# Performance work log

Measured on AMD Instinct MI355X. Metric: run time of the kernel, lower is better.

Reference implementation:

```python
import math
import jax, jax.numpy as jnp
import numpy as np

D_MODEL = 512
MAX_SEQ = 512
NUM_OUT = 16
H = 1  # num_heads


def _pos_encoding(d_model, seq_len):
    # sinusoidal PE, then flipped along the sequence axis (ReversedPositionalEncoding)
    pos = jnp.arange(seq_len, dtype=jnp.float32)[:, None]
    i = jnp.arange(0, d_model, 2, dtype=jnp.float32)
    ang = pos * jnp.exp(i * (-(math.log(10000.0) / d_model)))  # [S, d/2]
    pe = jnp.stack([jnp.sin(ang), jnp.cos(ang)], axis=-1).reshape(seq_len, d_model)
    return pe[::-1]


def _layernorm(x, w, b, eps=1e-5):
    m = jnp.mean(x, axis=-1, keepdims=True)
    v = jnp.mean(jnp.square(x - m), axis=-1, keepdims=True)
    return (x - m) / jnp.sqrt(v + eps) * w + b


def setup_inputs() -> dict:
    key = jax.random.key(0)
    ks = jax.random.split(key, 8)
    B = 128
    latents = jax.random.normal(ks[0], (B, D_MODEL, MAX_SEQ), dtype=jnp.float32)
    query_mask = jnp.ones((B, NUM_OUT), dtype=jnp.float32)
    query = 0.02 * jax.random.normal(ks[1], (NUM_OUT, D_MODEL), dtype=jnp.float32)
    return {
        "latents": latents,
        "query_mask": query_mask,
        "query": query,
        "ln_lat_w": jnp.ones((D_MODEL,), jnp.float32),
        "ln_lat_b": jnp.zeros((D_MODEL,), jnp.float32),
        "ln_q_w": jnp.ones((D_MODEL,), jnp.float32),
        "ln_q_b": jnp.zeros((D_MODEL,), jnp.float32),
        "Wq": 0.02 * jax.random.normal(ks[2], (D_MODEL, D_MODEL), jnp.float32),
        "bq": jnp.zeros((D_MODEL,), jnp.float32),
        "Wk": 0.02 * jax.random.normal(ks[3], (D_MODEL, D_MODEL), jnp.float32),
        "bk": jnp.zeros((D_MODEL,), jnp.float32),
        "Wv": 0.02 * jax.random.normal(ks[4], (D_MODEL, D_MODEL), jnp.float32),
        "bv": jnp.zeros((D_MODEL,), jnp.float32),
        "Wo": 0.02 * jax.random.normal(ks[5], (1, D_MODEL), jnp.float32),
        "bo": jnp.zeros((1,), jnp.float32),
    }


def reference(latents, query_mask, query, ln_lat_w, ln_lat_b, ln_q_w, ln_q_b,
              Wq, bq, Wk, bk, Wv, bv, Wo, bo):
    B, _, N = latents.shape  # latents: [B, d_model, N]
    scale = math.sqrt(D_MODEL)
    Dh = D_MODEL // H

    # cross-attention mask: query_mask [B,Nq] x all-ones latent mask [B,N]
    mask = jnp.einsum('bq,bk->bqk', query_mask, jnp.ones((B, N), latents.dtype))

    x = jnp.swapaxes(latents, 1, 2) * scale           # [B, N, d]
    x = x + _pos_encoding(D_MODEL, MAX_SEQ)[-N:]      # reversed PE, last N positions
    # dropout is identity in eval mode
    x = _layernorm(x, ln_lat_w, ln_lat_b)

    q = _layernorm(query * scale, ln_q_w, ln_q_b)     # [Nq, d]
    q = jnp.broadcast_to(q[None], (B, NUM_OUT, D_MODEL))

    qh = (q @ Wq.T + bq).reshape(B, NUM_OUT, H, Dh)
    kh = (x @ Wk.T + bk).reshape(B, N, H, Dh)
    vh = (x @ Wv.T + bv).reshape(B, N, H, Dh)

    scores = jnp.einsum('bqhd,bkhd->bhqk', qh, kh) / math.sqrt(Dh)
    scores = jnp.where(mask[:, None] == 0, -1e9, scores)
    attn_weights = jax.nn.softmax(scores, axis=-1)    # [B, H, Nq, N]

    attn = jnp.einsum('bhqk,bkhd->bqhd', attn_weights, vh).reshape(B, NUM_OUT, H * Dh)
    wipe = jnp.all(mask == 0, axis=2, keepdims=True)  # [B, Nq, 1]
    attn = jnp.where(wipe, 0.0, attn)

    logits = attn @ Wo.T + bo                         # [B, Nq, 1]
    return logits, attn_weights
```

## Files before the change

### kernel.cpp

```cpp
#include <hip/hip_runtime.h>
#include <math.h>

#define DM 512
#define NQ 16
#define NG (NQ + 1)
#define NR (NG + 3)

typedef __attribute__((ext_vector_type(2))) float f32x2;

__device__ __forceinline__ float wave_reduce_sum(float v) {
    #pragma unroll
    for (int off = 32; off > 0; off >>= 1) v += __shfl_xor(v, off, 64);
    return v;
}
__device__ __forceinline__ float wave_reduce_max(float v) {
    #pragma unroll
    for (int off = 32; off > 0; off >>= 1) v = fmaxf(v, __shfl_xor(v, off, 64));
    return v;
}

__global__ void k1_setup(const float* __restrict__ Wk, const float* __restrict__ Wv,
                         const float* __restrict__ query,
                         const float* __restrict__ ln_q_w, const float* __restrict__ ln_q_b,
                         float* __restrict__ PET, float* __restrict__ WkT,
                         float* __restrict__ WvT, float* __restrict__ q_ln, int N) {
    __shared__ float tile[64][65];
    int bx = blockIdx.x;
    int lane = threadIdx.x & 63;
    int w = threadIdx.x >> 6;

    if (bx < 128) {
        int ntile = bx & 7, jg = bx >> 3;
        int n = ntile * 64 + lane;
        float p = (float)(N - 1 - n);
        const float c = -logf(10000.f) / (float)DM;
        int jbase = jg * 16 + w * 4;
        #pragma unroll
        for (int u = 0; u < 4; ++u) {
            int j = jbase + u;
            float wj = expf((float)(2 * j) * c);
            float ang = p * wj;
            PET[(size_t)(2 * j) * N + n] = sinf(ang);
            PET[(size_t)(2 * j + 1) * N + n] = cosf(ang);
        }
    } else if (bx < 256) {
        int t = bx - 128;
        const float* W = (t >> 6) ? Wv : Wk;
        float* WT = (t >> 6) ? WvT : WkT;
        int tl = t & 63;
        int te = tl >> 3, td = tl & 7;
        #pragma unroll
        for (int i = 0; i < 16; ++i) {
            int el = w * 16 + i;
            tile[el][lane] = W[(size_t)(te * 64 + el) * DM + td * 64 + lane];
        }
        __syncthreads();
        #pragma unroll
        for (int i = 0; i < 16; ++i) {
            int dl = w * 16 + i;
            WT[(size_t)(td * 64 + dl) * DM + te * 64 + lane] = tile[lane][dl];
        }
    } else {
        const float scale = 22.627416997969522f;
        for (int qi = 0; qi < 4; ++qi) {
            int q = w * 4 + qi;
            float vals[8], s = 0.f, s2 = 0.f;
            #pragma unroll
            for (int i = 0; i < 8; ++i) {
                float x = query[q * DM + i * 64 + lane] * scale;
                vals[i] = x; s += x; s2 += x * x;
            }
            s = wave_reduce_sum(s); s2 = wave_reduce_sum(s2);
            float m = s * (1.f / DM);
            float var = s2 * (1.f / DM) - m * m;
            float rstd = rsqrtf(var + 1e-5f);
            #pragma unroll
            for (int i = 0; i < 8; ++i) {
                int d = i * 64 + lane;
                q_ln[q * DM + d] = (vals[i] - m) * rstd * ln_q_w[d] + ln_q_b[d];
            }
        }
    }
}

__global__ void k2_qh(const float* __restrict__ q_ln, const float* __restrict__ Wq,
                      const float* __restrict__ bq, float* __restrict__ qh) {
    int idx = blockIdx.x * 4 + (threadIdx.x >> 6);
    int lane = threadIdx.x & 63;
    int q = idx >> 9, e = idx & 511;
    const float4* wr = (const float4*)(Wq + (size_t)e * DM);
    const float4* xr = (const float4*)(q_ln + (size_t)q * DM);
    float4 w0 = wr[lane * 2], w1 = wr[lane * 2 + 1];
    float4 x0 = xr[lane * 2], x1 = xr[lane * 2 + 1];
    float s = w0.x * x0.x + w0.y * x0.y + w0.z * x0.z + w0.w * x0.w
            + w1.x * x1.x + w1.y * x1.y + w1.z * x1.z + w1.w * x1.w;
    s = wave_reduce_sum(s);
    if (lane == 0) qh[q * DM + e] = s + bq[e];
}

__global__ void k3_qt(const float* __restrict__ qh, const float* __restrict__ WkT,
                      const float* __restrict__ Wo, const float* __restrict__ WvT,
                      const float* __restrict__ lnw,
                      float* __restrict__ qt, float* __restrict__ A,
                      f32x2* __restrict__ A2, float* __restrict__ wvout) {
    int idx = blockIdx.x * 4 + (threadIdx.x >> 6);
    int lane = threadIdx.x & 63;
    int g = idx >> 9, d = idx & 511;
    const float4* wr;
    const float4* xr;
    if (g < NQ) {
        wr = (const float4*)(WkT + (size_t)d * DM);
        xr = (const float4*)(qh + (size_t)g * DM);
    } else {
        wr = (const float4*)(WvT + (size_t)d * DM);
        xr = (const float4*)Wo;
    }
    float4 w0 = wr[lane * 2], w1 = wr[lane * 2 + 1];
    float4 x0 = xr[lane * 2], x1 = xr[lane * 2 + 1];
    float s = w0.x * x0.x + w0.y * x0.y + w0.z * x0.z + w0.w * x0.w
            + w1.x * x1.x + w1.y * x1.y + w1.z * x1.z + w1.w * x1.w;
    s = wave_reduce_sum(s);
    if (lane == 0) {
        if (g < NQ) qt[g * DM + d] = s;
        else wvout[d] = s;
        float a = s * lnw[d];
        A[g * DM + d] = a;
        f32x2 ap; ap.x = a; ap.y = a;
        A2[g * DM + d] = ap;
    }
}

__global__ void k4_pea(const float* __restrict__ A, const float* __restrict__ PET,
                       const float* __restrict__ qt, const float* __restrict__ qh,
                       const float* __restrict__ wv, const float* __restrict__ lnb,
                       const float* __restrict__ bk, const float* __restrict__ Wo,
                       const float* __restrict__ bv,
                       float* __restrict__ peA, float* __restrict__ peS,
                       float* __restrict__ peQ, float* __restrict__ consts, int N) {
    __shared__ float red[4][64];
    int bx = blockIdx.x;
    int lane = threadIdx.x & 63;
    int w = threadIdx.x >> 6;

    if (bx < 152) {
        int g = bx >> 3, ntile = bx & 7;
        int n = ntile * 64 + lane;
        int d0 = w * 128;
        float acc = 0.f;
        if (g < NG) {
            for (int i = 0; i < 128; ++i) {
                int d = d0 + i;
                acc = fmaf(A[(size_t)g * DM + d], PET[(size_t)d * N + n], acc);
            }
        } else if (g == NG) {
            for (int i = 0; i < 128; ++i) acc += PET[(size_t)(d0 + i) * N + n];
        } else {
            for (int i = 0; i < 128; ++i) {
                float v = PET[(size_t)(d0 + i) * N + n];
                acc = fmaf(v, v, acc);
            }
        }
        red[w][lane] = acc;
        __syncthreads();
        if (w != 0) return;
        float tot = red[0][lane] + red[1][lane] + red[2][lane] + red[3][lane];
        if (g < NG) peA[(size_t)g * N + n] = tot;
        else if (g == NG) peS[n] = tot;
        else peQ[n] = tot;
    } else {
        int t = (bx - 152) * 4 + w;
        if (t > NQ) return;
        if (t < NQ) {
            float sa = 0.f, sc = 0.f, qb = 0.f;
            #pragma unroll
            for (int i = 0; i < 8; ++i) {
                int d = i * 64 + lane;
                sa += A[t * DM + d];
                sc = fmaf(qt[t * DM + d], lnb[d], sc);
                qb = fmaf(qh[t * DM + d], bk[d], qb);
            }
            sa = wave_reduce_sum(sa);
            sc = wave_reduce_sum(sc);
            qb = wave_reduce_sum(qb);
            if (lane == 0) { consts[t] = sa; consts[16 + t] = sc + qb; }
        } else {
            float sa = 0.f, cv = 0.f, bvo = 0.f;
            #pragma unroll
            for (int i = 0; i < 8; ++i) {
                int d = i * 64 + lane;
                sa += A[NQ * DM + d];
                cv = fmaf(wv[d], lnb[d], cv);
                bvo = fmaf(Wo[d], bv[d], bvo);
            }
            sa = wave_reduce_sum(sa);
            cv = wave_reduce_sum(cv);
            bvo = wave_reduce_sum(bvo);
            if (lane == 0) { consts[32] = sa; consts[33] = cv + bvo; }
        }
    }
}

__launch_bounds__(256, 4)
__global__ void main2_kernel(const float* __restrict__ latents,
                             const float* __restrict__ PET,
                             const f32x2* __restrict__ A2,
                             float* __restrict__ pbuf, int N) {
    int ntiles = N >> 7;
    int ntile = blockIdx.x % ntiles;
    int dh = blockIdx.x / ntiles;
    int b = blockIdx.y;
    int lane = threadIdx.x & 63;
    int w = threadIdx.x >> 6;
    int n0 = ntile * 128 + lane * 2;

    int d0 = __builtin_amdgcn_readfirstlane(dh * 256 + w * 64);
    const float* latf = latents + (size_t)b * DM * N + (size_t)d0 * N + n0;
    const float* petf = PET + (size_t)d0 * N + n0;

    f32x2 acc[NG];
    #pragma unroll
    for (int i = 0; i < NG; ++i) { acc[i].x = 0.f; acc[i].y = 0.f; }
    f32x2 S1 = {0.f, 0.f}, S2 = {0.f, 0.f}, Sx = {0.f, 0.f};

    const int U = 4;
    const int NC = 64 / U;
    f32x2 xb[2][U], pb[2][U];
    #pragma unroll
    for (int u = 0; u < U; ++u) {
        xb[0][u] = __builtin_nontemporal_load((const f32x2*)(latf + (size_t)u * N));
        pb[0][u] = *(const f32x2*)(petf + (size_t)u * N);
    }
    for (int c = 0; c < NC; c += 2) {
        #pragma unroll
        for (int u = 0; u < U; ++u) {
            size_t dd = (size_t)((c + 1) * U + u) * N;
            xb[1][u] = __builtin_nontemporal_load((const f32x2*)(latf + dd));
            pb[1][u] = *(const f32x2*)(petf + dd);
        }
        #pragma unroll
        for (int u = 0; u < U; ++u) {
            f32x2 x = xb[0][u], pe = pb[0][u];
            S1 += x; S2 += x * x; Sx += x * pe;
            int d = d0 + c * U + u;
            #pragma unroll
            for (int q = 0; q < NG; ++q)
                acc[q] += A2[(size_t)q * DM + d] * x;
        }
        if (c + 2 < NC) {
            #pragma unroll
            for (int u = 0; u < U; ++u) {
                size_t dd = (size_t)((c + 2) * U + u) * N;
                xb[0][u] = __builtin_nontemporal_load((const f32x2*)(latf + dd));
                pb[0][u] = *(const f32x2*)(petf + dd);
            }
        }
        #pragma unroll
        for (int u = 0; u < U; ++u) {
            f32x2 x = xb[1][u], pe = pb[1][u];
            S1 += x; S2 += x * x; Sx += x * pe;
            int d = d0 + (c + 1) * U + u;
            #pragma unroll
            for (int q = 0; q < NG; ++q)
                acc[q] += A2[(size_t)q * DM + d] * x;
        }
    }

    __shared__ f32x2 red[4][NR][64];
    red[w][0][lane] = S1;
    red[w][1][lane] = S2;
    red[w][2][lane] = Sx;
    #pragma unroll
    for (int i = 0; i < NG; ++i) red[w][3 + i][lane] = acc[i];
    __syncthreads();
    if (w != 0) return;

    float* pout = pbuf + (((size_t)dh * gridDim.y + b) * NR) * N + n0;
    #pragma unroll
    for (int i = 0; i < NR; ++i) {
        f32x2 t = red[0][i][lane] + red[1][i][lane] + red[2][i][lane] + red[3][i][lane];
        *(f32x2*)(pout + (size_t)i * N) = t;
    }
}

__global__ void finalize_kernel(const float* __restrict__ pbuf,
                                const float* __restrict__ peA,
                                const float* __restrict__ peS,
                                const float* __restrict__ peQ,
                                const float* __restrict__ consts,
                                float* __restrict__ scores,
                                float* __restrict__ vbuf, int N, int B) {
    int t = blockIdx.x * 256 + threadIdx.x;
    int ppb = N >> 1;
    int b = t / ppb;
    int n0 = (t - b * ppb) * 2;
    if (b >= B) return;
    const float scale = 22.627416997969522f;

    const float* p0 = pbuf + (((size_t)0 * B + b) * NR) * N + n0;
    const float* p1 = pbuf + (((size_t)1 * B + b) * NR) * N + n0;
    f32x2 tot[NR];
    #pragma unroll
    for (int i = 0; i < NR; ++i)
        tot[i] = *(const f32x2*)(p0 + (size_t)i * N) + *(const f32x2*)(p1 + (size_t)i * N);

    f32x2 peS2 = *(const f32x2*)(peS + n0);
    f32x2 peQ2 = *(const f32x2*)(peQ + n0);
    f32x2 m = (scale * tot[0] + peS2) * (1.f / DM);
    f32x2 ex2 = (scale * scale * tot[1] + 2.f * scale * tot[2] + peQ2) * (1.f / DM);
    f32x2 rstd;
    rstd.x = rsqrtf(ex2.x - m.x * m.x + 1e-5f);
    rstd.y = rsqrtf(ex2.y - m.y * m.y + 1e-5f);

    float sumAv = consts[32], CvT = consts[33];
    f32x2 peAv = *(const f32x2*)(peA + (size_t)NQ * N + n0);
    f32x2 v = rstd * (scale * tot[3 + NQ] + peAv - m * sumAv) + CvT;
    *(f32x2*)(vbuf + (size_t)b * N + n0) = v;

    const float isd = 0.044194173824159216f;
    #pragma unroll
    for (int q = 0; q < NQ; ++q) {
        f32x2 peAq = *(const f32x2*)(peA + (size_t)q * N + n0);
        f32x2 sc = (rstd * (scale * tot[3 + q] + peAq - m * consts[q])
                    + consts[16 + q]) * isd;
        *(f32x2*)(scores + ((size_t)b * NQ + q) * N + n0) = sc;
    }
}

__global__ void softmax_kernel(const float* __restrict__ scores,
                               const float* __restrict__ vbuf,
                               const float* __restrict__ query_mask,
                               const float* __restrict__ bo,
                               float* __restrict__ out_logits,
                               float* __restrict__ out_attn, int N) {
    int r = blockIdx.x * 4 + (threadIdx.x >> 6);
    int b = r >> 4;
    int lane = threadIdx.x & 63;
    float4* attn_row = (float4*)(out_attn + (size_t)r * N);
    float qm = query_mask[r];
    int nv = N / 4;
    if (qm == 0.f) {
        float u = 1.f / (float)N;
        float4 uv = make_float4(u, u, u, u);
        for (int i = lane; i < nv; i += 64) attn_row[i] = uv;
        if (lane == 0) out_logits[r] = bo[0];
        return;
    }
    const float4* srow = (const float4*)(scores + (size_t)r * N);
    float4 sv[2];
    sv[0] = srow[lane]; sv[1] = srow[64 + lane];
    float mx = fmaxf(fmaxf(fmaxf(sv[0].x, sv[0].y), fmaxf(sv[0].z, sv[0].w)),
                     fmaxf(fmaxf(sv[1].x, sv[1].y), fmaxf(sv[1].z, sv[1].w)));
    mx = wave_reduce_max(mx);
    float sum = 0.f;
    #pragma unroll
    for (int i = 0; i < 2; ++i) {
        sv[i].x = expf(sv[i].x - mx); sv[i].y = expf(sv[i].y - mx);
        sv[i].z = expf(sv[i].z - mx); sv[i].w = expf(sv[i].w - mx);
        sum += sv[i].x + sv[i].y + sv[i].z + sv[i].w;
    }
    sum = wave_reduce_sum(sum);
    float inv = 1.f / sum;
    const float4* vrow = (const float4*)(vbuf + (size_t)b * N);
    float lp = 0.f;
    #pragma unroll
    for (int i = 0; i < 2; ++i) {
        float4 vv = vrow[i * 64 + lane];
        float4 wgt;
        wgt.x = sv[i].x * inv; wgt.y = sv[i].y * inv;
        wgt.z = sv[i].z * inv; wgt.w = sv[i].w * inv;
        attn_row[i * 64 + lane] = wgt;
        lp += wgt.x * vv.x + wgt.y * vv.y + wgt.z * vv.z + wgt.w * vv.w;
    }
    lp = wave_reduce_sum(lp);
    if (lane == 0) out_logits[r] = lp + bo[0];
}

extern "C" void kernel_launch(void* const* d_in, const int* in_sizes, int n_in,
                              void* d_out, int out_size, void* d_ws, size_t ws_size,
                              hipStream_t stream) {
    const float* latents    = (const float*)d_in[0];
    const float* query_mask = (const float*)d_in[1];
    const float* query      = (const float*)d_in[2];
    const float* ln_lat_w   = (const float*)d_in[3];
    const float* ln_lat_b   = (const float*)d_in[4];
    const float* ln_q_w     = (const float*)d_in[5];
    const float* ln_q_b     = (const float*)d_in[6];
    const float* Wq         = (const float*)d_in[7];
    const float* bq         = (const float*)d_in[8];
    const float* Wk         = (const float*)d_in[9];
    const float* bk         = (const float*)d_in[10];
    const float* Wv         = (const float*)d_in[11];
    const float* bv         = (const float*)d_in[12];
    const float* Wo         = (const float*)d_in[13];
    const float* bo         = (const float*)d_in[14];

    int B = in_sizes[1] / NQ;
    int N = in_sizes[0] / (DM * B);

    float* ws = (float*)d_ws;
    size_t off = 0;
    float* PET    = ws + off; off += (size_t)DM * N;
    float* WkT    = ws + off; off += (size_t)DM * DM;
    float* WvT    = ws + off; off += (size_t)DM * DM;
    float* peS    = ws + off; off += N;
    float* peQ    = ws + off; off += N;
    float* q_ln   = ws + off; off += NQ * DM;
    float* qh     = ws + off; off += NQ * DM;
    float* qt     = ws + off; off += NQ * DM;
    float* A      = ws + off; off += NG * DM;
    float* A2     = ws + off; off += (size_t)NG * DM * 2;
    float* wv     = ws + off; off += DM;
    float* peA    = ws + off; off += (size_t)NG * N;
    float* consts = ws + off; off += 64;
    float* scores = ws + off; off += (size_t)B * NQ * N;
    float* vbuf   = ws + off; off += (size_t)B * N;
    float* pbuf   = ws + off; off += (size_t)2 * B * NR * N;

    float* out_logits = (float*)d_out;
    float* out_attn   = out_logits + (size_t)B * NQ;

    k1_setup<<<257, 256, 0, stream>>>(Wk, Wv, query, ln_q_w, ln_q_b,
                                      PET, WkT, WvT, q_ln, N);
    k2_qh<<<NQ * DM / 4, 256, 0, stream>>>(q_ln, Wq, bq, qh);
    k3_qt<<<NG * DM / 4, 256, 0, stream>>>(qh, WkT, Wo, WvT, ln_lat_w,
                                           qt, A, (f32x2*)A2, wv);
    k4_pea<<<157, 256, 0, stream>>>(A, PET, qt, qh, wv, ln_lat_b, bk, Wo, bv,
                                    peA, peS, peQ, consts, N);
    dim3 gmain((N >> 7) * 2, B);
    main2_kernel<<<gmain, 256, 0, stream>>>(latents, PET, (const f32x2*)A2,
                                            pbuf, N);
    int fin_threads = B * (N / 2);
    finalize_kernel<<<(fin_threads + 255) / 256, 256, 0, stream>>>(
        pbuf, peA, peS, peQ, consts, scores, vbuf, N, B);
    softmax_kernel<<<B * NQ / 4, 256, 0, stream>>>(scores, vbuf, query_mask, bo,
                                                   out_logits, out_attn, N);
}
```

Measured before the change: 254.9 us.

## Collapse pipeline into four kernels and fold positional encoding into main pass

Replaces the seven-kernel pipeline with four. Query layernorm is fused with the Wq projection, the weight transposes are dropped in favour of a column-wise GEMV, and the finalize and softmax stages are merged into one per-batch kernel that keeps scores in shared memory. The main kernel now adds scale*x+PE inline and splits d across 8 waves of a 512-thread block instead of two blocks, which removes the PE-side precompute and the cross-block partial sum. Risks include reduced parallelism in k_A (only 17 blocks) and higher register and shared-memory pressure in the main kernel.

Measured after the change: 278.7 us. 1.09x slower.

```diff
diff --git a/kernel.cpp b/kernel.cpp
--- a/kernel.cpp
+++ b/kernel.cpp
@@ -4,7 +4,7 @@
 #define DM 512
 #define NQ 16
 #define NG (NQ + 1)
-#define NR (NG + 3)
+#define NR (NG + 2)
 
 typedef __attribute__((ext_vector_type(2))) float f32x2;
 
@@ -19,18 +19,17 @@
     return v;
 }
 
-__global__ void k1_setup(const float* __restrict__ Wk, const float* __restrict__ Wv,
-                         const float* __restrict__ query,
-                         const float* __restrict__ ln_q_w, const float* __restrict__ ln_q_b,
-                         float* __restrict__ PET, float* __restrict__ WkT,
-                         float* __restrict__ WvT, float* __restrict__ q_ln, int N) {
-    __shared__ float tile[64][65];
+__global__ void k_setup(const float* __restrict__ query,
+                        const float* __restrict__ ln_q_w, const float* __restrict__ ln_q_b,
+                        const float* __restrict__ Wq, const float* __restrict__ bq,
+                        float* __restrict__ PET, float* __restrict__ qh, int N) {
+    int lane = threadIdx.x & 63;
     int bx = blockIdx.x;
-    int lane = threadIdx.x & 63;
-    int w = threadIdx.x >> 6;
-
-    if (bx < 128) {
-        int ntile = bx & 7, jg = bx >> 3;
+    int nt = N >> 6;
+    int petBlocks = nt * 16;
+    if (bx < petBlocks) {
+        int w = threadIdx.x >> 6;
+        int ntile = bx % nt, jg = bx / nt;
         int n = ntile * 64 + lane;
         float p = (float)(N - 1 - n);
         const float c = -logf(10000.f) / (float)DM;
@@ -43,184 +42,106 @@
             PET[(size_t)(2 * j) * N + n] = sinf(ang);
             PET[(size_t)(2 * j + 1) * N + n] = cosf(ang);
         }
-    } else if (bx < 256) {
-        int t = bx - 128;
-        const float* W = (t >> 6) ? Wv : Wk;
-        float* WT = (t >> 6) ? WvT : WkT;
-        int tl = t & 63;
-        int te = tl >> 3, td = tl & 7;
-        #pragma unroll
-        for (int i = 0; i < 16; ++i) {
-            int el = w * 16 + i;
-            tile[el][lane] = W[(size_t)(te * 64 + el) * DM + td * 64 + lane];
-        }
-        __syncthreads();
-        #pragma unroll
-        for (int i = 0; i < 16; ++i) {
-            int dl = w * 16 + i;
-            WT[(size_t)(td * 64 + dl) * DM + te * 64 + lane] = tile[lane][dl];
-        }
     } else {
+        int idx = (bx - petBlocks) * 4 + (threadIdx.x >> 6);
+        int q = idx >> 9, e = idx & 511;
         const float scale = 22.627416997969522f;
-        for (int qi = 0; qi < 4; ++qi) {
-            int q = w * 4 + qi;
-            float vals[8], s = 0.f, s2 = 0.f;
-            #pragma unroll
-            for (int i = 0; i < 8; ++i) {
-                float x = query[q * DM + i * 64 + lane] * scale;
-                vals[i] = x; s += x; s2 += x * x;
-            }
-            s = wave_reduce_sum(s); s2 = wave_reduce_sum(s2);
-            float m = s * (1.f / DM);
-            float var = s2 * (1.f / DM) - m * m;
-            float rstd = rsqrtf(var + 1e-5f);
-            #pragma unroll
-            for (int i = 0; i < 8; ++i) {
-                int d = i * 64 + lane;
-                q_ln[q * DM + d] = (vals[i] - m) * rstd * ln_q_w[d] + ln_q_b[d];
-            }
-        }
-    }
-}
-
-__global__ void k2_qh(const float* __restrict__ q_ln, const float* __restrict__ Wq,
-                      const float* __restrict__ bq, float* __restrict__ qh) {
-    int idx = blockIdx.x * 4 + (threadIdx.x >> 6);
-    int lane = threadIdx.x & 63;
-    int q = idx >> 9, e = idx & 511;
-    const float4* wr = (const float4*)(Wq + (size_t)e * DM);
-    const float4* xr = (const float4*)(q_ln + (size_t)q * DM);
-    float4 w0 = wr[lane * 2], w1 = wr[lane * 2 + 1];
-    float4 x0 = xr[lane * 2], x1 = xr[lane * 2 + 1];
-    float s = w0.x * x0.x + w0.y * x0.y + w0.z * x0.z + w0.w * x0.w
-            + w1.x * x1.x + w1.y * x1.y + w1.z * x1.z + w1.w * x1.w;
-    s = wave_reduce_sum(s);
-    if (lane == 0) qh[q * DM + e] = s + bq[e];
-}
-
-__global__ void k3_qt(const float* __restrict__ qh, const float* __restrict__ WkT,
-                      const float* __restrict__ Wo, const float* __restrict__ WvT,
-                      const float* __restrict__ lnw,
-                      float* __restrict__ qt, float* __restrict__ A,
-                      f32x2* __restrict__ A2, float* __restrict__ wvout) {
-    int idx = blockIdx.x * 4 + (threadIdx.x >> 6);
-    int lane = threadIdx.x & 63;
-    int g = idx >> 9, d = idx & 511;
-    const float4* wr;
-    const float4* xr;
-    if (g < NQ) {
-        wr = (const float4*)(WkT + (size_t)d * DM);
-        xr = (const float4*)(qh + (size_t)g * DM);
-    } else {
-        wr = (const float4*)(WvT + (size_t)d * DM);
-        xr = (const float4*)Wo;
-    }
-    float4 w0 = wr[lane * 2], w1 = wr[lane * 2 + 1];
-    float4 x0 = xr[lane * 2], x1 = xr[lane * 2 + 1];
-    float s = w0.x * x0.x + w0.y * x0.y + w0.z * x0.z + w0.w * x0.w
-            + w1.x * x1.x + w1.y * x1.y + w1.z * x1.z + w1.w * x1.w;
-    s = wave_reduce_sum(s);
-    if (lane == 0) {
-        if (g < NQ) qt[g * DM + d] = s;
-        else wvout[d] = s;
-        float a = s * lnw[d];
-        A[g * DM + d] = a;
-        f32x2 ap; ap.x = a; ap.y = a;
-        A2[g * DM + d] = ap;
-    }
-}
-
-__global__ void k4_pea(const float* __restrict__ A, const float* __restrict__ PET,
-                       const float* __restrict__ qt, const float* __restrict__ qh,
-                       const float* __restrict__ wv, const float* __restrict__ lnb,
-                       const float* __restrict__ bk, const float* __restrict__ Wo,
-                       const float* __restrict__ bv,
-                       float* __restrict__ peA, float* __restrict__ peS,
-                       float* __restrict__ peQ, float* __restrict__ consts, int N) {
-    __shared__ float red[4][64];
-    int bx = blockIdx.x;
-    int lane = threadIdx.x & 63;
-    int w = threadIdx.x >> 6;
-
-    if (bx < 152) {
-        int g = bx >> 3, ntile = bx & 7;
-        int n = ntile * 64 + lane;
-        int d0 = w * 128;
-        float acc = 0.f;
-        if (g < NG) {
-            for (int i = 0; i < 128; ++i) {
-                int d = d0 + i;
-                acc = fmaf(A[(size_t)g * DM + d], PET[(size_t)d * N + n], acc);
-            }
-        } else if (g == NG) {
-            for (int i = 0; i < 128; ++i) acc += PET[(size_t)(d0 + i) * N + n];
-        } else {
-            for (int i = 0; i < 128; ++i) {
-                float v = PET[(size_t)(d0 + i) * N + n];
-                acc = fmaf(v, v, acc);
-            }
-        }
-        red[w][lane] = acc;
-        __syncthreads();
-        if (w != 0) return;
-        float tot = red[0][lane] + red[1][lane] + red[2][lane] + red[3][lane];
-        if (g < NG) peA[(size_t)g * N + n] = tot;
-        else if (g == NG) peS[n] = tot;
-        else peQ[n] = tot;
-    } else {
-        int t = (bx - 152) * 4 + w;
-        if (t > NQ) return;
-        if (t < NQ) {
-            float sa = 0.f, sc = 0.f, qb = 0.f;
-            #pragma unroll
-            for (int i = 0; i < 8; ++i) {
-                int d = i * 64 + lane;
-                sa += A[t * DM + d];
-                sc = fmaf(qt[t * DM + d], lnb[d], sc);
-                qb = fmaf(qh[t * DM + d], bk[d], qb);
-            }
-            sa = wave_reduce_sum(sa);
-            sc = wave_reduce_sum(sc);
-            qb = wave_reduce_sum(qb);
-            if (lane == 0) { consts[t] = sa; consts[16 + t] = sc + qb; }
-        } else {
-            float sa = 0.f, cv = 0.f, bvo = 0.f;
-            #pragma unroll
-            for (int i = 0; i < 8; ++i) {
-                int d = i * 64 + lane;
-                sa += A[NQ * DM + d];
-                cv = fmaf(wv[d], lnb[d], cv);
-                bvo = fmaf(Wo[d], bv[d], bvo);
-            }
-            sa = wave_reduce_sum(sa);
-            cv = wave_reduce_sum(cv);
-            bvo = wave_reduce_sum(bvo);
-            if (lane == 0) { consts[32] = sa; consts[33] = cv + bvo; }
-        }
-    }
-}
-
-__launch_bounds__(256, 4)
-__global__ void main2_kernel(const float* __restrict__ latents,
+        const float4* qr = (const float4*)(query + (size_t)q * DM);
+        float4 a0 = qr[lane * 2], a1 = qr[lane * 2 + 1];
+        a0.x *= scale; a0.y *= scale; a0.z *= scale; a0.w *= scale;
+        a1.x *= scale; a1.y *= scale; a1.z *= scale; a1.w *= scale;
+        float s  = a0.x + a0.y + a0.z + a0.w + a1.x + a1.y + a1.z + a1.w;
+        float s2 = a0.x * a0.x + a0.y * a0.y + a0.z * a0.z + a0.w * a0.w
+                 + a1.x * a1.x + a1.y * a1.y + a1.z * a1.z + a1.w * a1.w;
+        s = wave_reduce_sum(s); s2 = wave_reduce_sum(s2);
+        float m = s * (1.f / DM);
+        float var = s2 * (1.f / DM) - m * m;
+        float rstd = rsqrtf(var + 1e-5f);
+        const float4* gw = (const float4*)ln_q_w;
+        const float4* gb = (const float4*)ln_q_b;
+        const float4* wr = (const float4*)(Wq + (size_t)e * DM);
+        float4 w0 = gw[lane * 2], w1 = gw[lane * 2 + 1];
+        float4 b0 = gb[lane * 2], b1 = gb[lane * 2 + 1];
+        float4 W0 = wr[lane * 2], W1 = wr[lane * 2 + 1];
+        float acc = ((a0.x - m) * rstd * w0.x + b0.x) * W0.x
+                  + ((a0.y - m) * rstd * w0.y + b0.y) * W0.y
+                  + ((a0.z - m) * rstd * w0.z + b0.z) * W0.z
+                  + ((a0.w - m) * rstd * w0.w + b0.w) * W0.w
+                  + ((a1.x - m) * rstd * w1.x + b1.x) * W1.x
+                  + ((a1.y - m) * rstd * w1.y + b1.y) * W1.y
+                  + ((a1.z - m) * rstd * w1.z + b1.z) * W1.z
+                  + ((a1.w - m) * rstd * w1.w + b1.w) * W1.w;
+        acc = wave_reduce_sum(acc);
+        if (lane == 0) qh[q * DM + e] = acc + bq[e];
+    }
+}
+
+__global__ void k_A(const float* __restrict__ qh, const float* __restrict__ Wk,
+                    const float* __restrict__ Wv, const float* __restrict__ Wo,
+                    const float* __restrict__ lnw, const float* __restrict__ lnb,
+                    const float* __restrict__ bk, const float* __restrict__ bv,
+                    f32x2* __restrict__ A2, float* __restrict__ consts) {
+    __shared__ float xrow[DM];
+    __shared__ float r4[3][4];
+    int g = blockIdx.x;
+    int tid = threadIdx.x;
+    int lane = tid & 63, w = tid >> 6;
+    const float* src = (g < NQ) ? (qh + (size_t)g * DM) : Wo;
+    for (int i = tid; i < DM; i += 256) xrow[i] = src[i];
+    __syncthreads();
+    const float* W = (g < NQ) ? Wk : Wv;
+    int d0 = tid, d1 = tid + 256;
+    float acc0 = 0.f, acc1 = 0.f;
+    #pragma unroll 8
+    for (int e = 0; e < DM; ++e) {
+        float xe = xrow[e];
+        acc0 = fmaf(W[(size_t)e * DM + d0], xe, acc0);
+        acc1 = fmaf(W[(size_t)e * DM + d1], xe, acc1);
+    }
+    float a0 = acc0 * lnw[d0], a1 = acc1 * lnw[d1];
+    f32x2 p0; p0.x = a0; p0.y = a0;
+    f32x2 p1; p1.x = a1; p1.y = a1;
+    A2[(size_t)g * DM + d0] = p0;
+    A2[(size_t)g * DM + d1] = p1;
+    const float* bvec = (g < NQ) ? bk : bv;
+    float sA = a0 + a1;
+    float sL = acc0 * lnb[d0] + acc1 * lnb[d1];
+    float sB = xrow[d0] * bvec[d0] + xrow[d1] * bvec[d1];
+    sA = wave_reduce_sum(sA);
+    sL = wave_reduce_sum(sL);
+    sB = wave_reduce_sum(sB);
+    if (lane == 0) { r4[0][w] = sA; r4[1][w] = sL; r4[2][w] = sB; }
+    __syncthreads();
+    if (tid == 0) {
+        float SA = r4[0][0] + r4[0][1] + r4[0][2] + r4[0][3];
+        float SL = r4[1][0] + r4[1][1] + r4[1][2] + r4[1][3];
+        float SB = r4[2][0] + r4[2][1] + r4[2][2] + r4[2][3];
+        if (g < NQ) { consts[g] = SA; consts[16 + g] = SL + SB; }
+        else        { consts[32] = SA; consts[33] = SL + SB; }
+    }
+}
+
+__launch_bounds__(512, 4)
+__global__ void main3_kernel(const float* __restrict__ latents,
                              const float* __restrict__ PET,
                              const f32x2* __restrict__ A2,
                              float* __restrict__ pbuf, int N) {
-    int ntiles = N >> 7;
-    int ntile = blockIdx.x % ntiles;
-    int dh = blockIdx.x / ntiles;
+    int ntile = blockIdx.x;
     int b = blockIdx.y;
     int lane = threadIdx.x & 63;
     int w = threadIdx.x >> 6;
     int n0 = ntile * 128 + lane * 2;
 
-    int d0 = __builtin_amdgcn_readfirstlane(dh * 256 + w * 64);
+    int d0 = __builtin_amdgcn_readfirstlane(w * 64);
     const float* latf = latents + (size_t)b * DM * N + (size_t)d0 * N + n0;
     const float* petf = PET + (size_t)d0 * N + n0;
+    const float scale = 22.627416997969522f;
+    f32x2 sc2; sc2.x = scale; sc2.y = scale;
 
     f32x2 acc[NG];
     #pragma unroll
     for (int i = 0; i < NG; ++i) { acc[i].x = 0.f; acc[i].y = 0.f; }
-    f32x2 S1 = {0.f, 0.f}, S2 = {0.f, 0.f}, Sx = {0.f, 0.f};
+    f32x2 S1 = {0.f, 0.f}, S2 = {0.f, 0.f};
 
     const int U = 4;
     const int NC = 64 / U;
@@ -239,12 +160,12 @@
         }
         #pragma unroll
         for (int u = 0; u < U; ++u) {
-            f32x2 x = xb[0][u], pe = pb[0][u];
-            S1 += x; S2 += x * x; Sx += x * pe;
+            f32x2 y = xb[0][u] * sc2 + pb[0][u];
+            S1 += y; S2 += y * y;
             int d = d0 + c * U + u;
             #pragma unroll
             for (int q = 0; q < NG; ++q)
-                acc[q] += A2[(size_t)q * DM + d] * x;
+                acc[q] += A2[(size_t)q * DM + d] * y;
         }
         if (c + 2 < NC) {
             #pragma unroll
@@ -256,123 +177,118 @@
         }
         #pragma unroll
         for (int u = 0; u < U; ++u) {
-            f32x2 x = xb[1][u], pe = pb[1][u];
-            S1 += x; S2 += x * x; Sx += x * pe;
+            f32x2 y = xb[1][u] * sc2 + pb[1][u];
+            S1 += y; S2 += y * y;
             int d = d0 + (c + 1) * U + u;
             #pragma unroll
             for (int q = 0; q < NG; ++q)
-                acc[q] += A2[(size_t)q * DM + d] * x;
+                acc[q] += A2[(size_t)q * DM + d] * y;
         }
     }
 
     __shared__ f32x2 red[4][NR][64];
-    red[w][0][lane] = S1;
-    red[w][1][lane] = S2;
-    red[w][2][lane] = Sx;
-    #pragma unroll
-    for (int i = 0; i < NG; ++i) red[w][3 + i][lane] = acc[i];
-    __syncthreads();
-    if (w != 0) return;
-
-    float* pout = pbuf + (((size_t)dh * gridDim.y + b) * NR) * N + n0;
-    #pragma unroll
-    for (int i = 0; i < NR; ++i) {
-        f32x2 t = red[0][i][lane] + red[1][i][lane] + red[2][i][lane] + red[3][i][lane];
-        *(f32x2*)(pout + (size_t)i * N) = t;
-    }
-}
-
-__global__ void finalize_kernel(const float* __restrict__ pbuf,
-                                const float* __restrict__ peA,
-                                const float* __restrict__ peS,
-                                const float* __restrict__ peQ,
-                                const float* __restrict__ consts,
-                                float* __restrict__ scores,
-                                float* __restrict__ vbuf, int N, int B) {
-    int t = blockIdx.x * 256 + threadIdx.x;
-    int ppb = N >> 1;
-    int b = t / ppb;
-    int n0 = (t - b * ppb) * 2;
-    if (b >= B) return;
-    const float scale = 22.627416997969522f;
-
-    const float* p0 = pbuf + (((size_t)0 * B + b) * NR) * N + n0;
-    const float* p1 = pbuf + (((size_t)1 * B + b) * NR) * N + n0;
-    f32x2 tot[NR];
-    #pragma unroll
-    for (int i = 0; i < NR; ++i)
-        tot[i] = *(const f32x2*)(p0 + (size_t)i * N) + *(const f32x2*)(p1 + (size_t)i * N);
-
-    f32x2 peS2 = *(const f32x2*)(peS + n0);
-    f32x2 peQ2 = *(const f32x2*)(peQ + n0);
-    f32x2 m = (scale * tot[0] + peS2) * (1.f / DM);
-    f32x2 ex2 = (scale * scale * tot[1] + 2.f * scale * tot[2] + peQ2) * (1.f / DM);
-    f32x2 rstd;
-    rstd.x = rsqrtf(ex2.x - m.x * m.x + 1e-5f);
-    rstd.y = rsqrtf(ex2.y - m.y * m.y + 1e-5f);
-
-    float sumAv = consts[32], CvT = consts[33];
-    f32x2 peAv = *(const f32x2*)(peA + (size_t)NQ * N + n0);
-    f32x2 v = rstd * (scale * tot[3 + NQ] + peAv - m * sumAv) + CvT;
-    *(f32x2*)(vbuf + (size_t)b * N + n0) = v;
-
+    if (w >= 4) {
+        int ww = w - 4;
+        red[ww][0][lane] = S1;
+        red[ww][1][lane] = S2;
+        #pragma unroll
+        for (int i = 0; i < NG; ++i) red[ww][2 + i][lane] = acc[i];
+    }
+    __syncthreads();
+    if (w < 4) {
+        red[w][0][lane] += S1;
+        red[w][1][lane] += S2;
+        #pragma unroll
+        for (int i = 0; i < NG; ++i) red[w][2 + i][lane] += acc[i];
+    }
+    __syncthreads();
+    if (w == 0) {
+        float* pout = pbuf + (size_t)b * NR * N + n0;
+        #pragma unroll
+        for (int i = 0; i < NR; ++i) {
+            f32x2 t = red[0][i][lane] + red[1][i][lane]
+                    + red[2][i][lane] + red[3][i][lane];
+            *(f32x2*)(pout + (size_t)i * N) = t;
+        }
+    }
+}
+
+__global__ void k_fin(const float* __restrict__ pbuf,
+                      const float* __restrict__ consts,
+                      const float* __restrict__ query_mask,
+                      const float* __restrict__ bo,
+                      float* __restrict__ out_logits,
+                      float* __restrict__ out_attn, int N) {
+    __shared__ float scs[NQ][512];
+    __shared__ float vls[512];
+    int b = blockIdx.x;
+    int tid = threadIdx.x;
     const float isd = 0.044194173824159216f;
-    #pragma unroll
-    for (int q = 0; q < NQ; ++q) {
-        f32x2 peAq = *(const f32x2*)(peA + (size_t)q * N + n0);
-        f32x2 sc = (rstd * (scale * tot[3 + q] + peAq - m * consts[q])
-                    + consts[16 + q]) * isd;
-        *(f32x2*)(scores + ((size_t)b * NQ + q) * N + n0) = sc;
-    }
-}
-
-__global__ void softmax_kernel(const float* __restrict__ scores,
-                               const float* __restrict__ vbuf,
-                               const float* __restrict__ query_mask,
-                               const float* __restrict__ bo,
-                               float* __restrict__ out_logits,
-                               float* __restrict__ out_attn, int N) {
-    int r = blockIdx.x * 4 + (threadIdx.x >> 6);
-    int b = r >> 4;
-    int lane = threadIdx.x & 63;
-    float4* attn_row = (float4*)(out_attn + (size_t)r * N);
-    float qm = query_mask[r];
-    int nv = N / 4;
-    if (qm == 0.f) {
-        float u = 1.f / (float)N;
-        float4 uv = make_float4(u, u, u, u);
-        for (int i = lane; i < nv; i += 64) attn_row[i] = uv;
-        if (lane == 0) out_logits[r] = bo[0];
-        return;
-    }
-    const float4* srow = (const float4*)(scores + (size_t)r * N);
-    float4 sv[2];
-    sv[0] = srow[lane]; sv[1] = srow[64 + lane];
-    float mx = fmaxf(fmaxf(fmaxf(sv[0].x, sv[0].y), fmaxf(sv[0].z, sv[0].w)),
-                     fmaxf(fmaxf(sv[1].x, sv[1].y), fmaxf(sv[1].z, sv[1].w)));
-    mx = wave_reduce_max(mx);
-    float sum = 0.f;
-    #pragma unroll
-    for (int i = 0; i < 2; ++i) {
-        sv[i].x = expf(sv[i].x - mx); sv[i].y = expf(sv[i].y - mx);
-        sv[i].z = expf(sv[i].z - mx); sv[i].w = expf(sv[i].w - mx);
-        sum += sv[i].x + sv[i].y + sv[i].z + sv[i].w;
-    }
-    sum = wave_reduce_sum(sum);
-    float inv = 1.f / sum;
-    const float4* vrow = (const float4*)(vbuf + (size_t)b * N);
-    float lp = 0.f;
-    #pragma unroll
-    for (int i = 0; i < 2; ++i) {
-        float4 vv = vrow[i * 64 + lane];
-        float4 wgt;
-        wgt.x = sv[i].x * inv; wgt.y = sv[i].y * inv;
-        wgt.z = sv[i].z * inv; wgt.w = sv[i].w * inv;
-        attn_row[i * 64 + lane] = wgt;
-        lp += wgt.x * vv.x + wgt.y * vv.y + wgt.z * vv.z + wgt.w * vv.w;
-    }
-    lp = wave_reduce_sum(lp);
-    if (lane == 0) out_logits[r] = lp + bo[0];
+    float c32 = consts[32], c33 = consts[33];
+
+    for (int np = tid; np < (N >> 1); np += 256) {
+        int n0 = np * 2;
+        const float* p = pbuf + (size_t)b * NR * N + n0;
+        f32x2 t[NR];
+        #pragma unroll
+        for (int i = 0; i < NR; ++i) t[i] = *(const f32x2*)(p + (size_t)i * N);
+        f32x2 m = t[0] * (1.f / DM);
+        f32x2 ex2 = t[1] * (1.f / DM);
+        f32x2 rstd;
+        rstd.x = rsqrtf(ex2.x - m.x * m.x + 1e-5f);
+        rstd.y = rsqrtf(ex2.y - m.y * m.y + 1e-5f);
+        f32x2 v = rstd * (t[2 + NQ] - m * c32) + c33;
+        *(f32x2*)&vls[n0] = v;
+        #pragma unroll
+        for (int q = 0; q < NQ; ++q) {
+            f32x2 sc = (rstd * (t[2 + q] - m * consts[q]) + consts[16 + q]) * isd;
+            *(f32x2*)&scs[q][n0] = sc;
+        }
+    }
+    __syncthreads();
+
+    int lane = tid & 63, w = tid >> 6;
+    int nv = N >> 2;
+    for (int q = w; q < NQ; q += 4) {
+        int r = b * NQ + q;
+        float qm = query_mask[r];
+        float4* arow = (float4*)(out_attn + (size_t)r * N);
+        if (qm == 0.f) {
+            float u = 1.f / (float)N;
+            float4 uv = make_float4(u, u, u, u);
+            for (int i = lane; i < nv; i += 64) arow[i] = uv;
+            if (lane == 0) out_logits[r] = bo[0];
+            continue;
+        }
+        const float4* srow = (const float4*)scs[q];
+        float4 sv[2];
+        sv[0] = srow[lane]; sv[1] = srow[64 + lane];
+        float mx = fmaxf(fmaxf(fmaxf(sv[0].x, sv[0].y), fmaxf(sv[0].z, sv[0].w)),
+                         fmaxf(fmaxf(sv[1].x, sv[1].y), fmaxf(sv[1].z, sv[1].w)));
+        mx = wave_reduce_max(mx);
+        float sum = 0.f;
+        #pragma unroll
+        for (int i = 0; i < 2; ++i) {
+            sv[i].x = expf(sv[i].x - mx); sv[i].y = expf(sv[i].y - mx);
+            sv[i].z = expf(sv[i].z - mx); sv[i].w = expf(sv[i].w - mx);
+            sum += sv[i].x + sv[i].y + sv[i].z + sv[i].w;
+        }
+        sum = wave_reduce_sum(sum);
+        float inv = 1.f / sum;
+        const float4* vrow = (const float4*)vls;
+        float lp = 0.f;
+        #pragma unroll
+        for (int i = 0; i < 2; ++i) {
+            float4 vv = vrow[i * 64 + lane];
+            float4 wgt;
+            wgt.x = sv[i].x * inv; wgt.y = sv[i].y * inv;
+            wgt.z = sv[i].z * inv; wgt.w = sv[i].w * inv;
+            arow[i * 64 + lane] = wgt;
+            lp += wgt.x * vv.x + wgt.y * vv.y + wgt.z * vv.z + wgt.w * vv.w;
+        }
+        lp = wave_reduce_sum(lp);
+        if (lane == 0) out_logits[r] = lp + bo[0];
+    }
 }
 
 extern "C" void kernel_launch(void* const* d_in, const int* in_sizes, int n_in,
@@ -400,38 +316,21 @@
     float* ws = (float*)d_ws;
     size_t off = 0;
     float* PET    = ws + off; off += (size_t)DM * N;
-    float* WkT    = ws + off; off += (size_t)DM * DM;
-    float* WvT    = ws + off; off += (size_t)DM * DM;
-    float* peS    = ws + off; off += N;
-    float* peQ    = ws + off; off += N;
-    float* q_ln   = ws + off; off += NQ * DM;
     float* qh     = ws + off; off += NQ * DM;
-    float* qt     = ws + off; off += NQ * DM;
-    float* A      = ws + off; off += NG * DM;
     float* A2     = ws + off; off += (size_t)NG * DM * 2;
-    float* wv     = ws + off; off += DM;
-    float* peA    = ws + off; off += (size_t)NG * N;
     float* consts = ws + off; off += 64;
-    float* scores = ws + off; off += (size_t)B * NQ * N;
-    float* vbuf   = ws + off; off += (size_t)B * N;
-    float* pbuf   = ws + off; off += (size_t)2 * B * NR * N;
+    float* pbuf   = ws + off; off += (size_t)B * NR * N;
 
     float* out_logits = (float*)d_out;
     float* out_attn   = out_logits + (size_t)B * NQ;
 
-    k1_setup<<<257, 256, 0, stream>>>(Wk, Wv, query, ln_q_w, ln_q_b,
-                                      PET, WkT, WvT, q_ln, N);
-    k2_qh<<<NQ * DM / 4, 256, 0, stream>>>(q_ln, Wq, bq, qh);
-    k3_qt<<<NG * DM / 4, 256, 0, stream>>>(qh, WkT, Wo, WvT, ln_lat_w,
-                                           qt, A, (f32x2*)A2, wv);
-    k4_pea<<<157, 256, 0, stream>>>(A, PET, qt, qh, wv, ln_lat_b, bk, Wo, bv,
-                                    peA, peS, peQ, consts, N);
-    dim3 gmain((N >> 7) * 2, B);
-    main2_kernel<<<gmain, 256, 0, stream>>>(latents, PET, (const f32x2*)A2,
-                                            pbuf, N);
-    int fin_threads = B * (N / 2);
-    finalize_kernel<<<(fin_threads + 255) / 256, 256, 0, stream>>>(
-        pbuf, peA, peS, peQ, consts, scores, vbuf, N, B);
-    softmax_kernel<<<B * NQ / 4, 256, 0, stream>>>(scores, vbuf, query_mask, bo,
-                                                   out_logits, out_attn, N);
-}
+    int petBlocks = (N >> 6) * 16;
+    k_setup<<<petBlocks + NQ * DM / 4, 256, 0, stream>>>(
+        query, ln_q_w, ln_q_b, Wq, bq, PET, qh, N);
+    k_A<<<NG, 256, 0, stream>>>(qh, Wk, Wv, Wo, ln_lat_w, ln_lat_b, bk, bv,
+                                (f32x2*)A2, consts);
+    main3_kernel<<<dim3(N >> 7, B), 512, 0, stream>>>(latents, PET,
+                                                      (const f32x2*)A2, pbuf, N);
+    k_fin<<<B, 256, 0, stream>>>(pbuf, consts, query_mask, bo,
+                                 out_logits, out_attn, N);
+}
```
